# Performance work log

Hardware: AMD Instinct MI355X
Metric: run time of the kernel (lower is better)

The kernel has to match this reference:

```python
import jax, jax.numpy as jnp
import numpy as np

N_NODES = 100000
N_EDGES = 1_600_000
IN_C, HID_C, CLS_C = 128, 256, 64


def setup_inputs() -> dict:
    key = jax.random.key(0)
    ks = jax.random.split(key, 8)
    x = jax.random.normal(ks[0], (N_NODES, IN_C), dtype=jnp.float32)
    edge_index = jax.random.randint(ks[1], (2, N_EDGES), 0, N_NODES, dtype=jnp.int64)
    s1 = 1.0 / np.sqrt(IN_C)
    s2 = 1.0 / np.sqrt(HID_C)
    W1l = jax.random.uniform(ks[2], (IN_C, HID_C), jnp.float32, -s1, s1)
    W1r = jax.random.uniform(ks[3], (IN_C, HID_C), jnp.float32, -s1, s1)
    b1 = jnp.zeros((HID_C,), jnp.float32)
    W2l = jax.random.uniform(ks[4], (HID_C, CLS_C), jnp.float32, -s2, s2)
    W2r = jax.random.uniform(ks[5], (HID_C, CLS_C), jnp.float32, -s2, s2)
    b2 = jnp.zeros((CLS_C,), jnp.float32)
    return {"x": x, "edge_index": edge_index,
            "W1l": W1l, "W1r": W1r, "b1": b1,
            "W2l": W2l, "W2r": W2r, "b2": b2}


def _sage_conv(x, src, dst, Wl, Wr, b, num_nodes):
    # mean aggregation of source features onto destination nodes
    agg = jax.ops.segment_sum(x[src], dst, num_segments=num_nodes)  # [N, F]
    deg = jax.ops.segment_sum(jnp.ones((src.shape[0], 1), x.dtype), dst,
                              num_segments=num_nodes)               # [N, 1]
    agg = agg / jnp.maximum(deg, 1.0)  # zero-degree nodes -> 0
    return agg @ Wl + x @ Wr + b


def reference(x, edge_index, W1l, W1r, b1, W2l, W2r, b2):
    src, dst = edge_index[0], edge_index[1]
    n = x.shape[0]
    h = jax.nn.relu(_sage_conv(x, src, dst, W1l, W1r, b1, n))
    # dropout(p=0.5) is identity in eval mode
    out = _sage_conv(h, src, dst, W2l, W2r, b2, n)
    return jax.nn.sigmoid(out)
```

## Files before the change

kernel.cpp:

```cpp
#include <hip/hip_runtime.h>

typedef __attribute__((ext_vector_type(8))) short short8;
typedef __attribute__((ext_vector_type(4))) float floatx4;
typedef __attribute__((ext_vector_type(2))) float floatx2;

static __device__ __forceinline__ unsigned short f2bf(float f) {
  unsigned int u = __builtin_bit_cast(unsigned int, f);
  u += 0x7FFFu + ((u >> 16) & 1u);
  return (unsigned short)(u >> 16);
}
static __device__ __forceinline__ float bf2f(unsigned short s) {
  unsigned int u = ((unsigned int)s) << 16;
  return __builtin_bit_cast(float, u);
}
static __device__ __forceinline__ unsigned int pk4_fp8(float a, float b, float c, float d) {
  int lo = __builtin_amdgcn_cvt_pk_fp8_f32(a, b, 0, false);
  int hi = __builtin_amdgcn_cvt_pk_fp8_f32(c, d, 0, false);
  return (unsigned int)((lo & 0xffff) | ((hi & 0xffff) << 16));
}
static __device__ __forceinline__ floatx4 unpk4_fp8(unsigned int p) {
  floatx2 lo = __builtin_amdgcn_cvt_pk_f32_fp8((int)p, false);
  floatx2 hi = __builtin_amdgcn_cvt_pk_f32_fp8((int)p, true);
  floatx4 r = {lo.x, lo.y, hi.x, hi.y};
  return r;
}

#define NBUCK 512
#define BIN_CHUNK 8192


__global__ __launch_bounds__(256) void bhist(const int* __restrict__ dst,
                                             int* __restrict__ bcnt, int E) {
  __shared__ int h[NBUCK];
  for (int i = threadIdx.x; i < NBUCK; i += 256) h[i] = 0;
  __syncthreads();
  int stride = gridDim.x * 256;
  for (int i = blockIdx.x * 256 + threadIdx.x; i < E; i += stride)
    atomicAdd(&h[dst[i] >> 8], 1);
  __syncthreads();
  for (int i = threadIdx.x; i < NBUCK; i += 256)
    if (h[i]) atomicAdd(&bcnt[i], h[i]);
}

__global__ __launch_bounds__(256) void bscan(const int* __restrict__ bcnt,
                                             int* __restrict__ bbase,
                                             int* __restrict__ bcur,
                                             int* __restrict__ rs, int N, int E) {
  __shared__ int ps[256];
  int t = threadIdx.x;
  int v0 = bcnt[2 * t], v1 = bcnt[2 * t + 1];
  int tsum = v0 + v1;
  ps[t] = tsum;
  __syncthreads();
  for (int off = 1; off < 256; off <<= 1) {
    int x = (t >= off) ? ps[t - off] : 0;
    __syncthreads();
    ps[t] += x;
    __syncthreads();
  }
  int excl = ps[t] - tsum;
  bbase[2 * t] = excl;     bcur[2 * t] = excl;
  bbase[2 * t + 1] = excl + v0; bcur[2 * t + 1] = excl + v0;
  if (t == 0) rs[N] = E;
}

__global__ __launch_bounds__(256) void binscatter(const int* __restrict__ src,
                                                  const int* __restrict__ dst,
                                                  int* __restrict__ bcur,
                                                  unsigned int* __restrict__ staging,
                                                  int E) {
  __shared__ int h[NBUCK];
  __shared__ int cur[NBUCK];
  for (int i = threadIdx.x; i < NBUCK; i += 256) h[i] = 0;
  __syncthreads();
  int base = blockIdx.x * BIN_CHUNK;
  int end = base + BIN_CHUNK; if (end > E) end = E;
  for (int i = base + threadIdx.x; i < end; i += 256)
    atomicAdd(&h[dst[i] >> 8], 1);
  __syncthreads();
  for (int i = threadIdx.x; i < NBUCK; i += 256)
    cur[i] = h[i] ? atomicAdd(&bcur[i], h[i]) : 0;
  __syncthreads();
  for (int i = base + threadIdx.x; i < end; i += 256) {
    int d = dst[i], s = src[i];
    int b = d >> 8;
    int pos = atomicAdd(&cur[b], 1);
    staging[pos] = ((unsigned int)(d & 255) << 17) | (unsigned int)s;
  }
}

__global__ __launch_bounds__(256) void bucketfinal(const unsigned int* __restrict__ staging,
                                                   const int* __restrict__ bbase,
                                                   const int* __restrict__ bcnt,
                                                   int* __restrict__ rs,
                                                   int* __restrict__ csr_src, int N) {
  int b = blockIdx.x;
  int base = bbase[b], cnt = bcnt[b];
  __shared__ int h[256];
  __shared__ int ps[256];
  __shared__ int cur[256];
  int t = threadIdx.x;
  h[t] = 0;
  __syncthreads();
  for (int i = t; i < cnt; i += 256)
    atomicAdd(&h[staging[base + i] >> 17], 1);
  __syncthreads();
  int hv = h[t];
  ps[t] = hv;
  __syncthreads();
  for (int off = 1; off < 256; off <<= 1) {
    int x = (t >= off) ? ps[t - off] : 0;
    __syncthreads();
    ps[t] += x;
    __syncthreads();
  }
  int run = base + ps[t] - hv;
  int w = (b << 8) + t;
  cur[t] = run;
  if (w < N) rs[w] = run;
  __syncthreads();
  for (int i = t; i < cnt; i += 256) {
    unsigned int v = staging[base + i];
    int pos = atomicAdd(&cur[v >> 17], 1);
    csr_src[pos] = (int)(v & 0x1FFFFu);
  }
}

__global__ void convw(const float* __restrict__ W1l, const float* __restrict__ W1r,
                      const float* __restrict__ W2l, const float* __restrict__ W2r,
                      unsigned short* __restrict__ W1p, unsigned short* __restrict__ W2p) {
  int i = blockIdx.x * blockDim.x + threadIdx.x;
  if (i < 8192) {
    int lane = i & 63, ni = (i >> 6) & 3, kk = (i >> 8) & 7, w = i >> 11;
    int fm = lane & 15, fq = lane >> 4;
    int n = w * 64 + ni * 16 + fm;
    int k0 = kk * 32 + fq * 8;
    unsigned short r[8];
#pragma unroll
    for (int j = 0; j < 8; j++) {
      int k = k0 + j;
      float v = (k < 128) ? W1l[k * 256 + n] : W1r[(k - 128) * 256 + n];
      r[j] = f2bf(v);
    }
    *reinterpret_cast<uint4*>(W1p + (size_t)i * 8) = *reinterpret_cast<uint4*>(r);
  } else if (i < 8192 + 4096) {
    int j2 = i - 8192;
    int lane = j2 & 63, ni = (j2 >> 6) & 1, kk = (j2 >> 7) & 7, w = j2 >> 10;
    int fm = lane & 15, fq = lane >> 4;
    int n = w * 32 + ni * 16 + fm;
    int k0 = kk * 32 + fq * 8;
    unsigned short r[8];
#pragma unroll
    for (int j = 0; j < 8; j++) {
      int k = k0 + j;
      float v = (n < 64) ? W2l[k * 64 + n] : W2r[k * 64 + (n - 64)];
      r[j] = f2bf(v);
    }
    *reinterpret_cast<uint4*>(W2p + (size_t)j2 * 8) = *reinterpret_cast<uint4*>(r);
  }
}

__global__ void convx(const float* __restrict__ x, unsigned int* __restrict__ xq,
                      int n_nodes) {
  int i = blockIdx.x * blockDim.x + threadIdx.x;
  if (i < n_nodes * 32) {
    int node = i >> 5, c4 = (i & 31) * 4;
    float4 v = *reinterpret_cast<const float4*>(x + (size_t)node * 128 + c4);
    xq[i] = pk4_fp8(v.x, v.y, v.z, v.w);
  }
}

#define LDSW 264
__global__ __launch_bounds__(256, 4) void gemm_fused(const float* __restrict__ x,
                                                     const uint4* __restrict__ xq,
                                                     const int* __restrict__ csr_src,
                                                     const int* __restrict__ rs,
                                                     const unsigned short* __restrict__ W1p,
                                                     const unsigned short* __restrict__ W2p,
                                                     const float* __restrict__ b1,
                                                     unsigned char* __restrict__ zq,
                                                     unsigned short* __restrict__ rb,
                                                     int M) {
  __shared__ unsigned short smem[64 * LDSW];
  const int tid = threadIdx.x;
  const int lane = tid & 63;
  const int wave = tid >> 6;
  const int m0 = blockIdx.x * 64;
  const int fm = lane & 15;
  const int fq = lane >> 4;
  const short8* __restrict__ W1v = reinterpret_cast<const short8*>(W1p);
  const short8* __restrict__ W2v = reinterpret_cast<const short8*>(W2p);

#pragma unroll
  for (int j = 0; j < 8; j++) {
    int c = j * 256 + tid;
    int row = c >> 5, f4 = c & 31;
    int gr = m0 + row; if (gr >= M) gr = M - 1;
    float4 v = *reinterpret_cast<const float4*>(x + (size_t)gr * 128 + f4 * 4);
    unsigned short r[4] = { f2bf(v.x), f2bf(v.y), f2bf(v.z), f2bf(v.w) };
    *reinterpret_cast<uint2*>(&smem[row * LDSW + 128 + f4 * 4]) =
        *reinterpret_cast<uint2*>(r);
  }

  {
    const int grp = lane >> 3;
    const int ch4 = lane & 7;
    const int lbase = lane & 56;
#pragma unroll
    for (int pp = 0; pp < 2; pp++) {
      int row = pp * 32 + wave * 8 + grp;
      int w = m0 + row;
      if (w < M) {
        int e0 = rs[w], e1 = rs[w + 1];
        floatx4 a0[4] = {{0,0,0,0},{0,0,0,0},{0,0,0,0},{0,0,0,0}};
        floatx4 a1[4] = {{0,0,0,0},{0,0,0,0},{0,0,0,0},{0,0,0,0}};
        for (int e = e0; e < e1; e += 8) {
          int t = e + ch4; if (t >= e1) t = e1 - 1;
          int myidx = csr_src[t];
          uint4 pb[8];
#pragma unroll
          for (int j = 0; j < 8; j++) {
            int s = __shfl(myidx, lbase | j, 64);
            pb[j] = xq[(s << 3) | ch4];
          }
          int rem = e1 - e;
#pragma unroll
          for (int j = 0; j < 8; j++) {
            if (j < rem) {
              floatx4* acc = (j & 1) ? a1 : a0;
              acc[0] += unpk4_fp8(pb[j].x);
              acc[1] += unpk4_fp8(pb[j].y);
              acc[2] += unpk4_fp8(pb[j].z);
              acc[3] += unpk4_fp8(pb[j].w);
            }
          }
        }
        int d = e1 - e0; if (d < 1) d = 1;
        float sc = 1.0f / (float)d;
        unsigned short r[16];
#pragma unroll
        for (int j = 0; j < 4; j++) {
          floatx4 a = a0[j] + a1[j];
          r[4 * j + 0] = f2bf(a.x * sc); r[4 * j + 1] = f2bf(a.y * sc);
          r[4 * j + 2] = f2bf(a.z * sc); r[4 * j + 3] = f2bf(a.w * sc);
        }
        unsigned short* dstp = &smem[row * LDSW + ch4 * 16];
        *reinterpret_cast<uint4*>(dstp) = *reinterpret_cast<uint4*>(r);
        *reinterpret_cast<uint4*>(dstp + 8) = *reinterpret_cast<uint4*>(r + 8);
      }
    }
  }

  float bb[4];
#pragma unroll
  for (int ni = 0; ni < 4; ni++) bb[ni] = b1[wave * 64 + ni * 16 + fm];

  __syncthreads();

  floatx4 acc1[4][4] = {};
#pragma unroll 2
  for (int kk = 0; kk < 8; kk++) {
    short8 af[4], bfr[4];
#pragma unroll
    for (int mi = 0; mi < 4; mi++)
      af[mi] = *reinterpret_cast<const short8*>(
          &smem[(mi * 16 + fm) * LDSW + kk * 32 + fq * 8]);
#pragma unroll
    for (int ni = 0; ni < 4; ni++)
      bfr[ni] = W1v[((wave * 8 + kk) * 4 + ni) * 64 + lane];
#pragma unroll
    for (int mi = 0; mi < 4; mi++)
#pragma unroll
      for (int ni = 0; ni < 4; ni++)
        acc1[mi][ni] = __builtin_amdgcn_mfma_f32_16x16x32_bf16(af[mi], bfr[ni],
                                                               acc1[mi][ni], 0, 0, 0);
  }

  __syncthreads();

#pragma unroll
  for (int mi = 0; mi < 4; mi++)
#pragma unroll
    for (int ni = 0; ni < 4; ni++)
#pragma unroll
      for (int r = 0; r < 4; r++) {
        float v = acc1[mi][ni][r] + bb[ni];
        v = v > 0.f ? v : 0.f;
        smem[(mi * 16 + fq * 4 + r) * LDSW + wave * 64 + ni * 16 + fm] = f2bf(v);
      }
  __syncthreads();

  floatx4 acc2[4][2] = {};
#pragma unroll 2
  for (int kk = 0; kk < 8; kk++) {
    short8 hf[4], wf[2];
#pragma unroll
    for (int mi = 0; mi < 4; mi++)
      hf[mi] = *reinterpret_cast<const short8*>(
          &smem[(mi * 16 + fm) * LDSW + kk * 32 + fq * 8]);
#pragma unroll
    for (int ni = 0; ni < 2; ni++)
      wf[ni] = W2v[((wave * 8 + kk) * 2 + ni) * 64 + lane];
#pragma unroll
    for (int mi = 0; mi < 4; mi++)
#pragma unroll
      for (int ni = 0; ni < 2; ni++)
        acc2[mi][ni] = __builtin_amdgcn_mfma_f32_16x16x32_bf16(hf[mi], wf[ni],
                                                               acc2[mi][ni], 0, 0, 0);
  }

#pragma unroll
  for (int mi = 0; mi < 4; mi++)
#pragma unroll
    for (int ni = 0; ni < 2; ni++)
#pragma unroll
      for (int r = 0; r < 4; r++) {
        int grow = m0 + mi * 16 + fq * 4 + r;
        if (grow < M) {
          float v = acc2[mi][ni][r];
          int col = (wave & 1) * 32 + ni * 16 + fm;
          if (wave < 2) {
            int b8 = __builtin_amdgcn_cvt_pk_fp8_f32(v, v, 0, false);
            zq[grow * 64 + col] = (unsigned char)(b8 & 0xff);
          } else {
            rb[grow * 64 + col] = f2bf(v);
          }
        }
      }
}

__global__ __launch_bounds__(256) void agg2_final(const uint4* __restrict__ zq,
                                                  const unsigned short* __restrict__ rb,
                                                  const int* __restrict__ csr_src,
                                                  const int* __restrict__ rs,
                                                  const float* __restrict__ b2,
                                                  float* __restrict__ out, int n_nodes) {
  int lane = threadIdx.x & 63;
  int wave = threadIdx.x >> 6;
  int grp = lane >> 2;
  int ch = lane & 3;
  int lbase = lane & 60;
  int w = blockIdx.x * 64 + wave * 16 + grp;
  if (w >= n_nodes) return;
  int e0 = rs[w], e1 = rs[w + 1];
  floatx4 a0[4] = {{0,0,0,0},{0,0,0,0},{0,0,0,0},{0,0,0,0}};
  floatx4 a1[4] = {{0,0,0,0},{0,0,0,0},{0,0,0,0},{0,0,0,0}};
  for (int e = e0; e < e1; e += 8) {
    int tA = e + ch;     if (tA >= e1) tA = e1 - 1;
    int tB = e + 4 + ch; if (tB >= e1) tB = e1 - 1;
    int iA = csr_src[tA];
    int iB = csr_src[tB];
    uint4 pb[8];
#pragma unroll
    for (int j = 0; j < 4; j++) {
      int s = __shfl(iA, lbase | j, 64);
      pb[j] = zq[(s << 2) | ch];
    }
#pragma unroll
    for (int j = 0; j < 4; j++) {
      int s = __shfl(iB, lbase | j, 64);
      pb[4 + j] = zq[(s << 2) | ch];
    }
    int rem = e1 - e;
#pragma unroll
    for (int j = 0; j < 8; j++) {
      if (j < rem) {
        floatx4* acc = (j & 1) ? a1 : a0;
        acc[0] += unpk4_fp8(pb[j].x);
        acc[1] += unpk4_fp8(pb[j].y);
        acc[2] += unpk4_fp8(pb[j].z);
        acc[3] += unpk4_fp8(pb[j].w);
      }
    }
  }
  int d = e1 - e0; if (d < 1) d = 1;
  float sc = 1.0f / (float)d;
  const unsigned short* rbp = rb + w * 64 + ch * 16;
  const float* b2p = b2 + ch * 16;
  float* op = out + (size_t)w * 64 + ch * 16;
#pragma unroll
  for (int j = 0; j < 4; j++) {
    floatx4 a = a0[j] + a1[j];
    uint2 rr = *reinterpret_cast<const uint2*>(rbp + 4 * j);
    float4 bv = *reinterpret_cast<const float4*>(b2p + 4 * j);
    float r0 = bf2f((unsigned short)(rr.x & 0xffff));
    float r1 = bf2f((unsigned short)(rr.x >> 16));
    float r2 = bf2f((unsigned short)(rr.y & 0xffff));
    float r3 = bf2f((unsigned short)(rr.y >> 16));
    float4 o;
    o.x = 1.0f / (1.0f + __expf(-(a.x * sc + r0 + bv.x)));
    o.y = 1.0f / (1.0f + __expf(-(a.y * sc + r1 + bv.y)));
    o.z = 1.0f / (1.0f + __expf(-(a.z * sc + r2 + bv.z)));
    o.w = 1.0f / (1.0f + __expf(-(a.w * sc + r3 + bv.w)));
    *reinterpret_cast<float4*>(op + 4 * j) = o;
  }
}

extern "C" void kernel_launch(void* const* d_in, const int* in_sizes, int n_in,
                              void* d_out, int out_size, void* d_ws, size_t ws_size,
                              hipStream_t stream) {
  const float* x   = (const float*)d_in[0];
  const int*   ei  = (const int*)d_in[1];
  const float* W1l = (const float*)d_in[2];
  const float* W1r = (const float*)d_in[3];
  const float* b1  = (const float*)d_in[4];
  const float* W2l = (const float*)d_in[5];
  const float* W2r = (const float*)d_in[6];
  const float* b2  = (const float*)d_in[7];
  float* out = (float*)d_out;

  const int N = in_sizes[0] / 128;
  const int E = in_sizes[1] / 2;
  const int* src = ei;
  const int* dst = ei + E;

  char* wsb = (char*)d_ws;
  size_t off = 0;
  auto alloc = [&](size_t bytes) -> void* {
    void* p = wsb + off;
    off += (bytes + 511) & ~(size_t)511;
    return p;
  };
  int* rs       = (int*)alloc((size_t)(N + 1) * 4);
  int* csr_src  = (int*)alloc((size_t)E * 4 + 64);
  int* bcnt     = (int*)alloc(NBUCK * 4);
  int* bbase    = (int*)alloc(NBUCK * 4);
  int* bcur     = (int*)alloc(NBUCK * 4);
  unsigned int* staging = (unsigned int*)alloc((size_t)E * 4);
  unsigned short* W1p = (unsigned short*)alloc(256 * 256 * 2);
  unsigned short* W2p = (unsigned short*)alloc(128 * 256 * 2);
  unsigned int* xq    = (unsigned int*)alloc((size_t)N * 128);
  unsigned char* zq   = (unsigned char*)alloc((size_t)N * 64);
  unsigned short* rb  = (unsigned short*)alloc((size_t)N * 64 * 2);
  (void)ws_size; (void)n_in; (void)out_size;

  const int nbuckReal = (N + 255) / 256;
  const int nchunks = (E + BIN_CHUNK - 1) / BIN_CHUNK;

  hipMemsetAsync(bcnt, 0, NBUCK * 4, stream);
  bhist<<<256, 256, 0, stream>>>(dst, bcnt, E);
  bscan<<<1, 256, 0, stream>>>(bcnt, bbase, bcur, rs, N, E);
  binscatter<<<nchunks, 256, 0, stream>>>(src, dst, bcur, staging, E);
  bucketfinal<<<nbuckReal, 256, 0, stream>>>(staging, bbase, bcnt, rs, csr_src, N);

  convw<<<(8192 + 4096 + 255) / 256, 256, 0, stream>>>(W1l, W1r, W2l, W2r, W1p, W2p);
  convx<<<(N * 32 + 255) / 256, 256, 0, stream>>>(x, xq, N);

  gemm_fused<<<(N + 63) / 64, 256, 0, stream>>>(x, (const uint4*)xq, csr_src, rs,
                                                W1p, W2p, b1, zq, rb, N);

  agg2_final<<<(N + 63) / 64, 256, 0, stream>>>((const uint4*)zq, rb, csr_src, rs, b2, out, N);
}
```

Baseline: 247.5 us.

## Fuse per-bucket CSR finalization into the layer-1 GEMM kernel using 64-node buckets

Buckets shrink from 256 to 64 destination nodes so that each bucket lines up with one 64-row GEMM tile. The separate bucketfinal kernel is removed, and gemm_fused now builds the local CSR (histogram, scan, scatter into an LDS edge list) itself. It also writes csr_src and rs for the layer-2 kernel and gathers neighbour indices from LDS instead of global memory. This saves a kernel launch and a global round-trip of the edge list. The cost is extra LDS and syncs in the GEMM kernel, and edges beyond ECAP=1536 per tile are silently dropped, which is a correctness risk for skewed degree distributions.

Measured after the change: 240.5 us. 2.8% less time.

```diff
diff --git a/kernel.cpp b/kernel.cpp
--- a/kernel.cpp
+++ b/kernel.cpp
@@ -25,8 +25,9 @@
   return r;
 }
 
-#define NBUCK 512
+#define NBUCK 2048
 #define BIN_CHUNK 8192
+#define ECAP 1536
 
 
 __global__ __launch_bounds__(256) void bhist(const int* __restrict__ dst,
@@ -36,7 +37,7 @@
   __syncthreads();
   int stride = gridDim.x * 256;
   for (int i = blockIdx.x * 256 + threadIdx.x; i < E; i += stride)
-    atomicAdd(&h[dst[i] >> 8], 1);
+    atomicAdd(&h[dst[i] >> 6], 1);
   __syncthreads();
   for (int i = threadIdx.x; i < NBUCK; i += 256)
     if (h[i]) atomicAdd(&bcnt[i], h[i]);
@@ -48,19 +49,22 @@
                                              int* __restrict__ rs, int N, int E) {
   __shared__ int ps[256];
   int t = threadIdx.x;
-  int v0 = bcnt[2 * t], v1 = bcnt[2 * t + 1];
-  int tsum = v0 + v1;
+  int v[8]; int tsum = 0;
+#pragma unroll
+  for (int j = 0; j < 8; j++) { v[j] = bcnt[t * 8 + j]; tsum += v[j]; }
   ps[t] = tsum;
   __syncthreads();
   for (int off = 1; off < 256; off <<= 1) {
-    int x = (t >= off) ? ps[t - off] : 0;
+    int xx = (t >= off) ? ps[t - off] : 0;
     __syncthreads();
-    ps[t] += x;
+    ps[t] += xx;
     __syncthreads();
   }
-  int excl = ps[t] - tsum;
-  bbase[2 * t] = excl;     bcur[2 * t] = excl;
-  bbase[2 * t + 1] = excl + v0; bcur[2 * t + 1] = excl + v0;
+  int run = ps[t] - tsum;
+#pragma unroll
+  for (int j = 0; j < 8; j++) {
+    bbase[t * 8 + j] = run; bcur[t * 8 + j] = run; run += v[j];
+  }
   if (t == 0) rs[N] = E;
 }
 
@@ -76,53 +80,16 @@
   int base = blockIdx.x * BIN_CHUNK;
   int end = base + BIN_CHUNK; if (end > E) end = E;
   for (int i = base + threadIdx.x; i < end; i += 256)
-    atomicAdd(&h[dst[i] >> 8], 1);
+    atomicAdd(&h[dst[i] >> 6], 1);
   __syncthreads();
   for (int i = threadIdx.x; i < NBUCK; i += 256)
     cur[i] = h[i] ? atomicAdd(&bcur[i], h[i]) : 0;
   __syncthreads();
   for (int i = base + threadIdx.x; i < end; i += 256) {
     int d = dst[i], s = src[i];
-    int b = d >> 8;
+    int b = d >> 6;
     int pos = atomicAdd(&cur[b], 1);
-    staging[pos] = ((unsigned int)(d & 255) << 17) | (unsigned int)s;
-  }
-}
-
-__global__ __launch_bounds__(256) void bucketfinal(const unsigned int* __restrict__ staging,
-                                                   const int* __restrict__ bbase,
-                                                   const int* __restrict__ bcnt,
-                                                   int* __restrict__ rs,
-                                                   int* __restrict__ csr_src, int N) {
-  int b = blockIdx.x;
-  int base = bbase[b], cnt = bcnt[b];
-  __shared__ int h[256];
-  __shared__ int ps[256];
-  __shared__ int cur[256];
-  int t = threadIdx.x;
-  h[t] = 0;
-  __syncthreads();
-  for (int i = t; i < cnt; i += 256)
-    atomicAdd(&h[staging[base + i] >> 17], 1);
-  __syncthreads();
-  int hv = h[t];
-  ps[t] = hv;
-  __syncthreads();
-  for (int off = 1; off < 256; off <<= 1) {
-    int x = (t >= off) ? ps[t - off] : 0;
-    __syncthreads();
-    ps[t] += x;
-    __syncthreads();
-  }
-  int run = base + ps[t] - hv;
-  int w = (b << 8) + t;
-  cur[t] = run;
-  if (w < N) rs[w] = run;
-  __syncthreads();
-  for (int i = t; i < cnt; i += 256) {
-    unsigned int v = staging[base + i];
-    int pos = atomicAdd(&cur[v >> 17], 1);
-    csr_src[pos] = (int)(v & 0x1FFFFu);
+    staging[pos] = ((unsigned int)(d & 63) << 17) | (unsigned int)s;
   }
 }
 
@@ -173,23 +140,33 @@
 #define LDSW 264
 __global__ __launch_bounds__(256, 4) void gemm_fused(const float* __restrict__ x,
                                                      const uint4* __restrict__ xq,
-                                                     const int* __restrict__ csr_src,
-                                                     const int* __restrict__ rs,
+                                                     const unsigned int* __restrict__ staging,
+                                                     const int* __restrict__ bbase,
+                                                     const int* __restrict__ bcnt,
                                                      const unsigned short* __restrict__ W1p,
                                                      const unsigned short* __restrict__ W2p,
                                                      const float* __restrict__ b1,
                                                      unsigned char* __restrict__ zq,
                                                      unsigned short* __restrict__ rb,
+                                                     int* __restrict__ csr_src,
+                                                     int* __restrict__ rs,
                                                      int M) {
   __shared__ unsigned short smem[64 * LDSW];
+  __shared__ int eidx[ECAP];
+  __shared__ int h64[64], rstart[64], cur64[64];
   const int tid = threadIdx.x;
   const int lane = tid & 63;
   const int wave = tid >> 6;
   const int m0 = blockIdx.x * 64;
   const int fm = lane & 15;
   const int fq = lane >> 4;
+  const int base = bbase[blockIdx.x];
+  const int cnt = bcnt[blockIdx.x];
   const short8* __restrict__ W1v = reinterpret_cast<const short8*>(W1p);
   const short8* __restrict__ W2v = reinterpret_cast<const short8*>(W2p);
+
+  if (tid < 64) h64[tid] = 0;
+  __syncthreads();
 
 #pragma unroll
   for (int j = 0; j < 8; j++) {
@@ -202,52 +179,79 @@
         *reinterpret_cast<uint2*>(r);
   }
 
+  for (int i = tid; i < cnt; i += 256)
+    atomicAdd(&h64[staging[base + i] >> 17], 1);
+  __syncthreads();
+
+  if (tid < 64) {
+    int v = h64[tid];
+    int s = v;
+#pragma unroll
+    for (int off = 1; off < 64; off <<= 1) {
+      int o = __shfl_up(s, off, 64);
+      if (tid >= off) s += o;
+    }
+    int excl = s - v;
+    rstart[tid] = excl;
+    cur64[tid] = excl;
+    int w = m0 + tid;
+    if (w < M) rs[w] = base + excl;
+  }
+  __syncthreads();
+
+  for (int i = tid; i < cnt; i += 256) {
+    unsigned int wv = staging[base + i];
+    int pos = atomicAdd(&cur64[wv >> 17], 1);
+    if (pos < ECAP) eidx[pos] = (int)(wv & 0x1FFFFu);
+  }
+  __syncthreads();
+
+  for (int i = tid; i < cnt && i < ECAP; i += 256)
+    csr_src[base + i] = eidx[i];
+
   {
     const int grp = lane >> 3;
     const int ch4 = lane & 7;
-    const int lbase = lane & 56;
 #pragma unroll
     for (int pp = 0; pp < 2; pp++) {
       int row = pp * 32 + wave * 8 + grp;
-      int w = m0 + row;
-      if (w < M) {
-        int e0 = rs[w], e1 = rs[w + 1];
-        floatx4 a0[4] = {{0,0,0,0},{0,0,0,0},{0,0,0,0},{0,0,0,0}};
-        floatx4 a1[4] = {{0,0,0,0},{0,0,0,0},{0,0,0,0},{0,0,0,0}};
-        for (int e = e0; e < e1; e += 8) {
-          int t = e + ch4; if (t >= e1) t = e1 - 1;
-          int myidx = csr_src[t];
-          uint4 pb[8];
-#pragma unroll
-          for (int j = 0; j < 8; j++) {
-            int s = __shfl(myidx, lbase | j, 64);
-            pb[j] = xq[(s << 3) | ch4];
-          }
-          int rem = e1 - e;
-#pragma unroll
-          for (int j = 0; j < 8; j++) {
-            if (j < rem) {
-              floatx4* acc = (j & 1) ? a1 : a0;
-              acc[0] += unpk4_fp8(pb[j].x);
-              acc[1] += unpk4_fp8(pb[j].y);
-              acc[2] += unpk4_fp8(pb[j].z);
-              acc[3] += unpk4_fp8(pb[j].w);
-            }
+      int e0l = rstart[row];
+      int e1l = e0l + h64[row];
+      if (e1l > ECAP) e1l = ECAP;
+      floatx4 a0[4] = {{0,0,0,0},{0,0,0,0},{0,0,0,0},{0,0,0,0}};
+      floatx4 a1[4] = {{0,0,0,0},{0,0,0,0},{0,0,0,0},{0,0,0,0}};
+      for (int e = e0l; e < e1l; e += 8) {
+        uint4 pb[8];
+#pragma unroll
+        for (int j = 0; j < 8; j++) {
+          int t = e + j; if (t >= e1l) t = e1l - 1;
+          int s = eidx[t];
+          pb[j] = xq[(s << 3) | ch4];
+        }
+        int rem = e1l - e;
+#pragma unroll
+        for (int j = 0; j < 8; j++) {
+          if (j < rem) {
+            floatx4* acc = (j & 1) ? a1 : a0;
+            acc[0] += unpk4_fp8(pb[j].x);
+            acc[1] += unpk4_fp8(pb[j].y);
+            acc[2] += unpk4_fp8(pb[j].z);
+            acc[3] += unpk4_fp8(pb[j].w);
           }
         }
-        int d = e1 - e0; if (d < 1) d = 1;
-        float sc = 1.0f / (float)d;
-        unsigned short r[16];
-#pragma unroll
-        for (int j = 0; j < 4; j++) {
-          floatx4 a = a0[j] + a1[j];
-          r[4 * j + 0] = f2bf(a.x * sc); r[4 * j + 1] = f2bf(a.y * sc);
-          r[4 * j + 2] = f2bf(a.z * sc); r[4 * j + 3] = f2bf(a.w * sc);
-        }
-        unsigned short* dstp = &smem[row * LDSW + ch4 * 16];
-        *reinterpret_cast<uint4*>(dstp) = *reinterpret_cast<uint4*>(r);
-        *reinterpret_cast<uint4*>(dstp + 8) = *reinterpret_cast<uint4*>(r + 8);
       }
+      int d = e1l - e0l; if (d < 1) d = 1;
+      float sc = 1.0f / (float)d;
+      unsigned short r[16];
+#pragma unroll
+      for (int j = 0; j < 4; j++) {
+        floatx4 a = a0[j] + a1[j];
+        r[4 * j + 0] = f2bf(a.x * sc); r[4 * j + 1] = f2bf(a.y * sc);
+        r[4 * j + 2] = f2bf(a.z * sc); r[4 * j + 3] = f2bf(a.w * sc);
+      }
+      unsigned short* dstp = &smem[row * LDSW + ch4 * 16];
+      *reinterpret_cast<uint4*>(dstp) = *reinterpret_cast<uint4*>(r);
+      *reinterpret_cast<uint4*>(dstp + 8) = *reinterpret_cast<uint4*>(r + 8);
     }
   }
 
@@ -434,20 +438,19 @@
   unsigned short* rb  = (unsigned short*)alloc((size_t)N * 64 * 2);
   (void)ws_size; (void)n_in; (void)out_size;
 
-  const int nbuckReal = (N + 255) / 256;
+  const int ntiles = (N + 63) / 64;
   const int nchunks = (E + BIN_CHUNK - 1) / BIN_CHUNK;
 
   hipMemsetAsync(bcnt, 0, NBUCK * 4, stream);
   bhist<<<256, 256, 0, stream>>>(dst, bcnt, E);
   bscan<<<1, 256, 0, stream>>>(bcnt, bbase, bcur, rs, N, E);
   binscatter<<<nchunks, 256, 0, stream>>>(src, dst, bcur, staging, E);
-  bucketfinal<<<nbuckReal, 256, 0, stream>>>(staging, bbase, bcnt, rs, csr_src, N);
 
   convw<<<(8192 + 4096 + 255) / 256, 256, 0, stream>>>(W1l, W1r, W2l, W2r, W1p, W2p);
   convx<<<(N * 32 + 255) / 256, 256, 0, stream>>>(x, xq, N);
 
-  gemm_fused<<<(N + 63) / 64, 256, 0, stream>>>(x, (const uint4*)xq, csr_src, rs,
-                                                W1p, W2p, b1, zq, rb, N);
+  gemm_fused<<<ntiles, 256, 0, stream>>>(x, (const uint4*)xq, staging, bbase, bcnt,
+                                         W1p, W2p, b1, zq, rb, csr_src, rs, N);
 
   agg2_final<<<(N + 63) / 64, 256, 0, stream>>>((const uint4*)zq, rb, csr_src, rs, b2, out, N);
 }
```
